# Kernel optimization log

Hardware: AMD Instinct MI355X
Metric: run time of the kernel (lower is better)

## Reference

```python
import jax, jax.numpy as jnp
import numpy as np

IN_CH = 256
HID = 64
HEADS = 3 * 0 + 4  # num_heads


def setup_inputs() -> dict:
    key = jax.random.key(0)
    ks = jax.random.split(key, 5)
    B, C, H, W = 2, IN_CH, 64, 64
    x = jax.random.normal(ks[0], (B, C, H, W), dtype=jnp.float32)
    # per-head embed conv (kernel 1 -> stored as [heads, 3*HID, C]); kaiming fan_out-ish scale
    w_embed = jax.random.normal(ks[1], (HEADS, 3 * HID, C), dtype=jnp.float32) * np.float32(np.sqrt(2.0 / (3 * HID)))
    b_embed = jnp.zeros((HEADS, 3 * HID), dtype=jnp.float32)
    # output ConvTranspose2d(hidden*heads -> C, kernel 1): weight [hidden*heads, C]
    w_out = jax.random.normal(ks[2], (HEADS * HID, C), dtype=jnp.float32) * np.float32(np.sqrt(2.0 / C))
    b_out = jnp.zeros((C,), dtype=jnp.float32)
    return {"x": x, "w_embed": w_embed, "b_embed": b_embed, "w_out": w_out, "b_out": b_out}


def reference(x, w_embed, b_embed, w_out, b_out):
    B, C, H, W = x.shape
    N = H * W
    nH = w_embed.shape[0]
    D = w_embed.shape[1] // 3
    scale = D ** -0.5
    # 1x1 embed conv per head: [B, nH, 3D, N]
    xf = x.reshape(B, C, N)
    qkv = jnp.einsum('bcn,hdc->bhdn', xf, w_embed) + b_embed[None, :, :, None]
    q, k, v = jnp.split(qkv, 3, axis=2)  # each [B, nH, D, N]
    attn = jnp.einsum('bhci,bhcj->bhij', q, k) * scale  # [B, nH, N, N]
    attn = jax.nn.softmax(attn, axis=-1)
    y = jnp.einsum('bhij,bhcj->bhci', attn, v)  # [B, nH, D, N]
    y = y.reshape(B, nH * D, N)
    # output 1x1 transposed conv (kernel 1 == plain 1x1 projection)
    out = jnp.einsum('bkn,kc->bcn', y, w_out) + b_out[None, :, None]
    out = out.reshape(B, C, H, W)
    return out + x  # residual
```

## Files before the change

### kernel.cpp

```cpp
#include <hip/hip_runtime.h>
#include <hip/hip_bf16.h>

#define NH   4
#define D_   64
#define N_   4096
#define C_   256
#define ME   768
#define QSCALE 0.18033688f

typedef float    f32x4  __attribute__((ext_vector_type(4)));
typedef float    f32x16 __attribute__((ext_vector_type(16)));
typedef _Float16 f16x8  __attribute__((ext_vector_type(8)));
typedef _Float16 f16x4  __attribute__((ext_vector_type(4)));
typedef unsigned int u32x2 __attribute__((ext_vector_type(2)));

#if defined(__has_builtin)
#if __has_builtin(__builtin_amdgcn_permlane32_swap)
#define HAVE_PERMLANE32_SWAP 1
#endif
#endif

__global__ __launch_bounds__(256) void prep_kernel(const float* __restrict__ x,
                                                   const float* __restrict__ w_out,
                                                   _Float16* __restrict__ xT,
                                                   _Float16* __restrict__ w_outT) {
    __shared__ float T[64][68];
    const int t = threadIdx.x, bx = blockIdx.x;
    if (bx < 512) {
        const int n0 = (bx & 63) * 64, c0 = ((bx >> 6) & 3) * 64, b = bx >> 8;
        const float* xp = x + ((size_t)b * C_ + c0) * N_ + n0;
        #pragma unroll
        for (int r = 0; r < 4; ++r) {
            int idx = r * 256 + t;
            int c = idx >> 4, ng = (idx & 15) * 4;
            *(f32x4*)&T[c][ng] = *(const f32x4*)(xp + (size_t)c * N_ + ng);
        }
        __syncthreads();
        _Float16* dp = xT + ((size_t)b * N_ + n0) * C_ + c0;
        #pragma unroll
        for (int r = 0; r < 2; ++r) {
            int idx = r * 256 + t;
            int n = idx >> 3, cg = (idx & 7) * 8;
            f16x8 v;
            #pragma unroll
            for (int j = 0; j < 8; ++j) v[j] = (_Float16)T[cg + j][n];
            *(f16x8*)(dp + (size_t)n * C_ + cg) = v;
        }
    } else {
        int tile = bx - 512;
        int tc = tile & 3, tk = tile >> 2;
        #pragma unroll
        for (int r = 0; r < 4; ++r) {
            int idx = r * 256 + t;
            int kl = idx >> 4, cl = (idx & 15) * 4;
            *(f32x4*)&T[kl][cl] = *(const f32x4*)(w_out + (size_t)(tk * 64 + kl) * C_ + tc * 64 + cl);
        }
        __syncthreads();
        #pragma unroll
        for (int r = 0; r < 2; ++r) {
            int idx = r * 256 + t;
            int cl = idx >> 3, kg = (idx & 7) * 8;
            f16x8 v;
            #pragma unroll
            for (int j = 0; j < 8; ++j) v[j] = (_Float16)T[kg + j][cl];
            *(f16x8*)(w_outT + (size_t)(tc * 64 + cl) * C_ + tk * 64 + kg) = v;
        }
    }
}

__global__ __launch_bounds__(256) void qkv_gemm(const _Float16* __restrict__ xT,
                                                const float* __restrict__ w_embed,
                                                const float* __restrict__ b_embed,
                                                _Float16* __restrict__ qT,
                                                _Float16* __restrict__ kT,
                                                _Float16* __restrict__ vB) {
    __shared__ __align__(16) union SM {
        struct { _Float16 A[64][40], X[64][40]; } s;
        float Os[64][68];
    } sm;
    const int n0 = blockIdx.x * 64, mt = blockIdx.y, b = blockIdx.z;
    const int m0 = mt * 64;
    const int t = threadIdx.x;
    const int lane = t & 63, w = t >> 6, quad = lane >> 4, l16 = lane & 15;
    const int srow = t >> 2, skoff = (t & 3) * 8;
    const int h = mt / 3, r3 = mt - h * 3;
    const float oscale = (r3 == 0) ? QSCALE : 1.0f;
    const float* ap = w_embed + (size_t)(m0 + srow) * C_ + skoff;
    const _Float16* xp = xT + ((size_t)b * N_ + n0 + srow) * C_ + skoff;
    f32x4 a0pre = *(const f32x4*)(ap);
    f32x4 a1pre = *(const f32x4*)(ap + 4);
    f16x8 xpre  = *(const f16x8*)(xp);
    f32x4 acc[4] = {};
    for (int k0 = 0; k0 < C_; k0 += 32) {
        __syncthreads();
        {
            f16x8 av = { (_Float16)a0pre[0], (_Float16)a0pre[1], (_Float16)a0pre[2], (_Float16)a0pre[3],
                         (_Float16)a1pre[0], (_Float16)a1pre[1], (_Float16)a1pre[2], (_Float16)a1pre[3] };
            *(f16x8*)&sm.s.A[srow][skoff] = av;
            *(f16x8*)&sm.s.X[srow][skoff] = xpre;
        }
        __syncthreads();
        if (k0 + 32 < C_) {
            a0pre = *(const f32x4*)(ap + k0 + 32);
            a1pre = *(const f32x4*)(ap + k0 + 36);
            xpre  = *(const f16x8*)(xp + k0 + 32);
        }
        f16x8 af = *(const f16x8*)&sm.s.A[w * 16 + l16][quad * 8];
        #pragma unroll
        for (int nb = 0; nb < 4; ++nb) {
            f16x8 bf = *(const f16x8*)&sm.s.X[nb * 16 + l16][quad * 8];
            acc[nb] = __builtin_amdgcn_mfma_f32_16x16x32_f16(af, bf, acc[nb], 0, 0, 0);
        }
    }
    float bias[4];
    #pragma unroll
    for (int rg = 0; rg < 4; ++rg) bias[rg] = b_embed[m0 + w * 16 + quad * 4 + rg];
    __syncthreads();
    #pragma unroll
    for (int nb = 0; nb < 4; ++nb)
        #pragma unroll
        for (int rg = 0; rg < 4; ++rg)
            sm.Os[w * 16 + quad * 4 + rg][nb * 16 + l16] = (acc[nb][rg] + bias[rg]) * oscale;
    __syncthreads();
    const int bh = b * NH + h;
    if (r3 < 2) {
        _Float16* dst = (r3 ? kT : qT) + ((size_t)bh * N_ + n0) * D_;
        #pragma unroll
        for (int r = 0; r < 2; ++r) {
            int idx = r * 256 + t;
            int n = idx >> 3, mg = (idx & 7) * 8;
            f16x8 v;
            #pragma unroll
            for (int j = 0; j < 8; ++j) v[j] = (_Float16)sm.Os[mg + j][n];
            *(f16x8*)(dst + (size_t)n * D_ + mg) = v;
        }
    } else {
        _Float16* dst = vB + (size_t)bh * D_ * N_ + n0;
        #pragma unroll
        for (int r = 0; r < 2; ++r) {
            int idx = r * 256 + t;
            int d = idx >> 3, ng = (idx & 7) * 8;
            f32x4 a = *(const f32x4*)&sm.Os[d][ng];
            f32x4 b2 = *(const f32x4*)&sm.Os[d][ng + 4];
            f16x8 v = { (_Float16)a[0], (_Float16)a[1], (_Float16)a[2], (_Float16)a[3],
                        (_Float16)b2[0], (_Float16)b2[1], (_Float16)b2[2], (_Float16)b2[3] };
            *(f16x8*)(dst + (size_t)d * N_ + ng) = v;
        }
    }
}

__global__ __launch_bounds__(256, 4) void attn_kernel(const _Float16* __restrict__ qT,
                                                      const _Float16* __restrict__ kT,
                                                      const _Float16* __restrict__ vB,
                                                      _Float16* __restrict__ opart,
                                                      float* __restrict__ mpart,
                                                      float* __restrict__ lpart,
                                                      int splog) {
    __shared__ __align__(16) union SM {
        struct { _Float16 K[2][64][76], V[2][64][76]; } s;
        _Float16 Os[128][76];
    } sm;
    const int t = threadIdx.x;
    const int nsp = 1 << splog;
    const int qt = blockIdx.x, h = blockIdx.y;
    const int b = blockIdx.z >> splog, s = blockIdx.z & (nsp - 1);
    const int bh = b * NH + h, sbh = s * 8 + bh;
    const _Float16* kp = kT + (size_t)bh * N_ * D_;
    const _Float16* vp = vB + (size_t)bh * D_ * N_;
    const int lane = t & 63, w = t >> 6, l32 = lane & 31, hl = lane >> 5;
    const int srow = t >> 3, scol = (t & 7) * 8;

    const _Float16* qp = qT + ((size_t)bh * N_ + qt * 128 + w * 32 + l32) * D_;
    f16x8 qf[4];
    #pragma unroll
    for (int kc = 0; kc < 4; ++kc) qf[kc] = *(const f16x8*)(qp + kc * 16 + hl * 8);

    f32x16 oacc0 = {}, oacc1 = {};
    float m_run = 0.f, l_run = 0.f;

    const int niter = 64 >> splog;
    const int jt_lo = s * niter, jt_hi = jt_lo + niter;
    f16x8 kpre[2], vpre[2];
    #pragma unroll
    for (int r = 0; r < 2; ++r) {
        int row = srow + r * 32;
        kpre[r] = *(const f16x8*)(kp + (size_t)(jt_lo * 64 + row) * D_ + scol);
        vpre[r] = *(const f16x8*)(vp + (size_t)row * N_ + jt_lo * 64 + scol);
    }

    int buf = 0;
    for (int jt = jt_lo; jt < jt_hi; ++jt, buf ^= 1) {
        #pragma unroll
        for (int r = 0; r < 2; ++r) {
            int row = srow + r * 32;
            *(f16x8*)&sm.s.K[buf][row][scol] = kpre[r];
            *(f16x8*)&sm.s.V[buf][row][scol] = vpre[r];
        }
        __syncthreads();
        if (jt + 1 < jt_hi) {
            #pragma unroll
            for (int r = 0; r < 2; ++r) {
                int row = srow + r * 32;
                kpre[r] = *(const f16x8*)(kp + (size_t)((jt + 1) * 64 + row) * D_ + scol);
                vpre[r] = *(const f16x8*)(vp + (size_t)row * N_ + (jt + 1) * 64 + scol);
            }
        }
        f32x16 sa0 = {}, sa1 = {};
        __builtin_amdgcn_s_setprio(1);
        #pragma unroll
        for (int kc = 0; kc < 4; ++kc) {
            f16x8 kf0 = *(const f16x8*)&sm.s.K[buf][l32][kc * 16 + hl * 8];
            sa0 = __builtin_amdgcn_mfma_f32_32x32x16_f16(kf0, qf[kc], sa0, 0, 0, 0);
            f16x8 kf1 = *(const f16x8*)&sm.s.K[buf][32 + l32][kc * 16 + hl * 8];
            sa1 = __builtin_amdgcn_mfma_f32_32x32x16_f16(kf1, qf[kc], sa1, 0, 0, 0);
        }
        __builtin_amdgcn_s_setprio(0);
        if (jt == jt_lo) {
            f32x16 mm;
            #pragma unroll
            for (int r = 0; r < 16; ++r) mm[r] = fmaxf(sa0[r], sa1[r]);
            f32x4 m4;
            #pragma unroll
            for (int r = 0; r < 4; ++r)
                m4[r] = fmaxf(fmaxf(mm[r], mm[r + 4]), fmaxf(mm[r + 8], mm[r + 12]));
            float mx = fmaxf(fmaxf(m4[0], m4[1]), fmaxf(m4[2], m4[3]));
            mx = fmaxf(mx, __shfl_xor(mx, 32));
            m_run = mx + 8.0f;
        }
        #pragma unroll
        for (int r = 0; r < 16; ++r) sa0[r] = __builtin_amdgcn_exp2f(sa0[r] - m_run);
        #pragma unroll
        for (int r = 0; r < 16; ++r) sa1[r] = __builtin_amdgcn_exp2f(sa1[r] - m_run);
        f32x16 sv = sa0 + sa1;
        f32x4 s4;
        #pragma unroll
        for (int r = 0; r < 4; ++r) s4[r] = (sv[r] + sv[r + 4]) + (sv[r + 8] + sv[r + 12]);
        float rs = (s4[0] + s4[1]) + (s4[2] + s4[3]);
        rs += __shfl_xor(rs, 32);
        l_run += rs;
#ifdef HAVE_PERMLANE32_SWAP
        #pragma unroll
        for (int jb = 0; jb < 2; ++jb) {
            const f32x16& sa = jb ? sa1 : sa0;
            #pragma unroll
            for (int kk = 0; kk < 2; ++kk) {
                unsigned int pa = __builtin_bit_cast(unsigned int,
                    __builtin_amdgcn_cvt_pkrtz(sa[kk * 8 + 0], sa[kk * 8 + 1]));
                unsigned int pb = __builtin_bit_cast(unsigned int,
                    __builtin_amdgcn_cvt_pkrtz(sa[kk * 8 + 2], sa[kk * 8 + 3]));
                unsigned int pc = __builtin_bit_cast(unsigned int,
                    __builtin_amdgcn_cvt_pkrtz(sa[kk * 8 + 4], sa[kk * 8 + 5]));
                unsigned int pd = __builtin_bit_cast(unsigned int,
                    __builtin_amdgcn_cvt_pkrtz(sa[kk * 8 + 6], sa[kk * 8 + 7]));
                u32x2 r0 = __builtin_amdgcn_permlane32_swap(pa, pc, false, false);
                u32x2 r1 = __builtin_amdgcn_permlane32_swap(pb, pd, false, false);
                union PF { unsigned int u[4]; f16x8 v; } pf;
                pf.u[0] = r0[0]; pf.u[1] = r1[0]; pf.u[2] = r0[1]; pf.u[3] = r1[1];
                const int vcol = jb * 32 + kk * 16 + hl * 8;
                f16x8 va  = *(const f16x8*)&sm.s.V[buf][l32][vcol];
                f16x8 vb2 = *(const f16x8*)&sm.s.V[buf][32 + l32][vcol];
                __builtin_amdgcn_s_setprio(1);
                oacc0 = __builtin_amdgcn_mfma_f32_32x32x16_f16(va, pf.v, oacc0, 0, 0, 0);
                oacc1 = __builtin_amdgcn_mfma_f32_32x32x16_f16(vb2, pf.v, oacc1, 0, 0, 0);
                __builtin_amdgcn_s_setprio(0);
            }
        }
#else
        #pragma unroll
        for (int jb = 0; jb < 2; ++jb) {
            const f32x16& sa = jb ? sa1 : sa0;
            union BU { f16x4 v; int d[2]; } bf[4];
            #pragma unroll
            for (int q = 0; q < 8; ++q)
                bf[q >> 1].d[q & 1] =
                    __builtin_bit_cast(int, __builtin_amdgcn_cvt_pkrtz(sa[2 * q], sa[2 * q + 1]));
            #pragma unroll
            for (int c = 0; c < 4; ++c) {
                const int vcol = jb * 32 + c * 8 + hl * 4;
                f16x4 va = *(const f16x4*)&sm.s.V[buf][l32][vcol];
                oacc0 = __builtin_amdgcn_mfma_f32_32x32x8f16(va, bf[c].v, oacc0, 0, 0, 0);
                f16x4 vb = *(const f16x4*)&sm.s.V[buf][32 + l32][vcol];
                oacc1 = __builtin_amdgcn_mfma_f32_32x32x8f16(vb, bf[c].v, oacc1, 0, 0, 0);
            }
        }
#endif
    }
    float linv = 1.f / l_run;
    if (hl == 0) {
        mpart[(size_t)sbh * N_ + qt * 128 + w * 32 + l32] = m_run;
        lpart[(size_t)sbh * N_ + qt * 128 + w * 32 + l32] = l_run;
    }
    __syncthreads();
    #pragma unroll
    for (int db = 0; db < 2; ++db) {
        const f32x16& oc = db ? oacc1 : oacc0;
        #pragma unroll
        for (int rq = 0; rq < 4; ++rq) {
            f16x4 pv = { (_Float16)(oc[rq * 4 + 0] * linv), (_Float16)(oc[rq * 4 + 1] * linv),
                         (_Float16)(oc[rq * 4 + 2] * linv), (_Float16)(oc[rq * 4 + 3] * linv) };
            *(f16x4*)&sm.Os[w * 32 + l32][db * 32 + rq * 8 + hl * 4] = pv;
        }
    }
    __syncthreads();
    _Float16* op = opart + ((size_t)sbh * N_ + qt * 128) * D_;
    #pragma unroll
    for (int r = 0; r < 4; ++r) {
        int idx = r * 256 + t;
        int i = idx >> 3, ch = (idx & 7) * 8;
        *(f16x8*)(op + (size_t)i * D_ + ch) = *(const f16x8*)&sm.Os[i][ch];
    }
}

__global__ __launch_bounds__(256) void projc_gemm(const _Float16* __restrict__ opart,
                                                  const float* __restrict__ mpart,
                                                  const float* __restrict__ lpart,
                                                  const _Float16* __restrict__ w_outT,
                                                  const float* __restrict__ b_out,
                                                  const float* __restrict__ x,
                                                  float* __restrict__ out) {
    __shared__ __align__(16) union SMP {
        struct {
            _Float16 Y[64][264];
            union { float W[4][64][4]; _Float16 A[128][40]; } u;
        } p;
        float Os[128][68];
    } sm;
    const int nt = blockIdx.x, chh = blockIdx.y, b = blockIdx.z;
    const int n0 = nt * 64, c0 = chh * 128;
    const int t = threadIdx.x;
    const int lane = t & 63, w = t >> 6, quad = lane >> 4, l16 = lane & 15;

    {
        const int nl = t & 63, hh = t >> 6;
        const int bh = b * NH + hh;
        float mv[4], lv[4];
        #pragma unroll
        for (int sI = 0; sI < 4; ++sI) {
            mv[sI] = mpart[(size_t)(sI * 8 + bh) * N_ + n0 + nl];
            lv[sI] = lpart[(size_t)(sI * 8 + bh) * N_ + n0 + nl];
        }
        float M = fmaxf(fmaxf(mv[0], mv[1]), fmaxf(mv[2], mv[3]));
        float ws[4], sum = 0.f;
        #pragma unroll
        for (int sI = 0; sI < 4; ++sI) {
            ws[sI] = __builtin_amdgcn_exp2f(mv[sI] - M) * lv[sI];
            sum += ws[sI];
        }
        float inv = 1.f / sum;
        #pragma unroll
        for (int sI = 0; sI < 4; ++sI) sm.p.u.W[hh][nl][sI] = ws[sI] * inv;
    }
    __syncthreads();

    #pragma unroll
    for (int it = 0; it < 8; ++it) {
        int idx = it * 256 + t;
        int n = idx >> 5, kg = (idx & 31) * 8;
        int hh = kg >> 6, d0 = kg & 63;
        const int bh = b * NH + hh;
        const float* Wn = &sm.p.u.W[hh][n][0];
        float accf[8] = {};
        #pragma unroll
        for (int sI = 0; sI < 4; ++sI) {
            f16x8 ov = *(const f16x8*)(opart + ((size_t)(sI * 8 + bh) * N_ + n0 + n) * D_ + d0);
            float wsv = Wn[sI];
            #pragma unroll
            for (int j = 0; j < 8; ++j) accf[j] += wsv * (float)ov[j];
        }
        f16x8 yv;
        #pragma unroll
        for (int j = 0; j < 8; ++j) yv[j] = (_Float16)accf[j];
        *(f16x8*)&sm.p.Y[n][kg] = yv;
    }
    __syncthreads();

    const int srow = t >> 1, skoff = (t & 1) * 16;
    const _Float16* ap = w_outT + (size_t)(c0 + srow) * C_ + skoff;
    f16x8 apre0 = *(const f16x8*)(ap);
    f16x8 apre1 = *(const f16x8*)(ap + 8);
    f32x4 acc[2][4] = {};
    for (int k0 = 0; k0 < C_; k0 += 32) {
        __syncthreads();
        *(f16x8*)&sm.p.u.A[srow][skoff]     = apre0;
        *(f16x8*)&sm.p.u.A[srow][skoff + 8] = apre1;
        __syncthreads();
        if (k0 + 32 < C_) {
            apre0 = *(const f16x8*)(ap + k0 + 32);
            apre1 = *(const f16x8*)(ap + k0 + 40);
        }
        #pragma unroll
        for (int cb = 0; cb < 2; ++cb) {
            f16x8 af = *(const f16x8*)&sm.p.u.A[w * 32 + cb * 16 + l16][quad * 8];
            #pragma unroll
            for (int nb = 0; nb < 4; ++nb) {
                f16x8 bf = *(const f16x8*)&sm.p.Y[nb * 16 + l16][k0 + quad * 8];
                acc[cb][nb] = __builtin_amdgcn_mfma_f32_16x16x32_f16(af, bf, acc[cb][nb], 0, 0, 0);
            }
        }
    }
    float bias[2][4];
    #pragma unroll
    for (int cb = 0; cb < 2; ++cb)
        #pragma unroll
        for (int rg = 0; rg < 4; ++rg)
            bias[cb][rg] = b_out[c0 + w * 32 + cb * 16 + quad * 4 + rg];
    __syncthreads();
    #pragma unroll
    for (int cb = 0; cb < 2; ++cb)
        #pragma unroll
        for (int nb = 0; nb < 4; ++nb)
            #pragma unroll
            for (int rg = 0; rg < 4; ++rg)
                sm.Os[w * 32 + cb * 16 + quad * 4 + rg][nb * 16 + l16] =
                    acc[cb][nb][rg] + bias[cb][rg];
    __syncthreads();
    const float* xp = x + ((size_t)b * C_ + c0) * N_ + n0;
    float* op = out + ((size_t)b * C_ + c0) * N_ + n0;
    #pragma unroll
    for (int r = 0; r < 8; ++r) {
        int idx = r * 256 + t;
        int c = idx >> 4, ng = (idx & 15) * 4;
        f32x4 v  = *(const f32x4*)&sm.Os[c][ng];
        f32x4 xv = *(const f32x4*)(xp + (size_t)c * N_ + ng);
        f32x4 o  = { v[0] + xv[0], v[1] + xv[1], v[2] + xv[2], v[3] + xv[3] };
        *(f32x4*)(op + (size_t)c * N_ + ng) = o;
    }
}

extern "C" void kernel_launch(void* const* d_in, const int* in_sizes, int n_in,
                              void* d_out, int out_size, void* d_ws, size_t ws_size,
                              hipStream_t stream) {
    const float* x       = (const float*)d_in[0];
    const float* w_embed = (const float*)d_in[1];
    const float* b_embed = (const float*)d_in[2];
    const float* w_out   = (const float*)d_in[3];
    const float* b_out   = (const float*)d_in[4];
    float* out = (float*)d_out;

    const int splog = 2;

    _Float16* base   = (_Float16*)d_ws;
    _Float16* xT     = base;
    _Float16* w_outT = base + 2293760;
    _Float16* qT     = base + 2359296;
    _Float16* kT     = base + 4456448;
    _Float16* vB     = base + 6553600;
    _Float16* opart  = base + 8650752;
    float*    mpart  = (float*)(opart + (size_t)4 * 8 * N_ * D_);
    float*    lpart  = mpart + (size_t)4 * 8 * N_;

    prep_kernel<<<dim3(528, 1, 1), 256, 0, stream>>>(x, w_out, xT, w_outT);
    qkv_gemm   <<<dim3(64, 12, 2), 256, 0, stream>>>(xT, w_embed, b_embed, qT, kT, vB);
    attn_kernel<<<dim3(32, 4, 2 << splog), 256, 0, stream>>>(qT, kT, vB, opart, mpart, lpart, splog);
    projc_gemm <<<dim3(64, 2, 2),  256, 0, stream>>>(opart, mpart, lpart, w_outT, b_out, x, out);
}
```

Measured before the change: 149.2 us.

## Single-buffer attention LDS, drop setprio, and allow 8-way KV split

The attention kernel's K/V shared-memory tiles go from double-buffered to single-buffered, with an extra barrier before each tile store. This roughly halves LDS use per block, which could let more blocks run at once per CU. The s_setprio hints around the MFMA sections are removed. When the workspace is large enough, the KV dimension is split 8 ways instead of 4, doubling attention grid parallelism, and the projection kernel is templated on the split count to merge more partial results. The extra barrier, the lost load/compute overlap and the larger partial-output traffic could offset these gains.

```diff
diff --git a/kernel.cpp b/kernel.cpp
--- a/kernel.cpp
+++ b/kernel.cpp
@@ -157,7 +157,7 @@
                                                       float* __restrict__ lpart,
                                                       int splog) {
     __shared__ __align__(16) union SM {
-        struct { _Float16 K[2][64][76], V[2][64][76]; } s;
+        struct { _Float16 K[64][76], V[64][76]; } s;
         _Float16 Os[128][76];
     } sm;
     const int t = threadIdx.x;
@@ -188,13 +188,13 @@
         vpre[r] = *(const f16x8*)(vp + (size_t)row * N_ + jt_lo * 64 + scol);
     }
 
-    int buf = 0;
-    for (int jt = jt_lo; jt < jt_hi; ++jt, buf ^= 1) {
+    for (int jt = jt_lo; jt < jt_hi; ++jt) {
+        __syncthreads();
         #pragma unroll
         for (int r = 0; r < 2; ++r) {
             int row = srow + r * 32;
-            *(f16x8*)&sm.s.K[buf][row][scol] = kpre[r];
-            *(f16x8*)&sm.s.V[buf][row][scol] = vpre[r];
+            *(f16x8*)&sm.s.K[row][scol] = kpre[r];
+            *(f16x8*)&sm.s.V[row][scol] = vpre[r];
         }
         __syncthreads();
         if (jt + 1 < jt_hi) {
@@ -206,15 +206,13 @@
             }
         }
         f32x16 sa0 = {}, sa1 = {};
-        __builtin_amdgcn_s_setprio(1);
         #pragma unroll
         for (int kc = 0; kc < 4; ++kc) {
-            f16x8 kf0 = *(const f16x8*)&sm.s.K[buf][l32][kc * 16 + hl * 8];
+            f16x8 kf0 = *(const f16x8*)&sm.s.K[l32][kc * 16 + hl * 8];
             sa0 = __builtin_amdgcn_mfma_f32_32x32x16_f16(kf0, qf[kc], sa0, 0, 0, 0);
-            f16x8 kf1 = *(const f16x8*)&sm.s.K[buf][32 + l32][kc * 16 + hl * 8];
+            f16x8 kf1 = *(const f16x8*)&sm.s.K[32 + l32][kc * 16 + hl * 8];
             sa1 = __builtin_amdgcn_mfma_f32_32x32x16_f16(kf1, qf[kc], sa1, 0, 0, 0);
         }
-        __builtin_amdgcn_s_setprio(0);
         if (jt == jt_lo) {
             f32x16 mm;
             #pragma unroll
@@ -257,12 +255,10 @@
                 union PF { unsigned int u[4]; f16x8 v; } pf;
                 pf.u[0] = r0[0]; pf.u[1] = r1[0]; pf.u[2] = r0[1]; pf.u[3] = r1[1];
                 const int vcol = jb * 32 + kk * 16 + hl * 8;
-                f16x8 va  = *(const f16x8*)&sm.s.V[buf][l32][vcol];
-                f16x8 vb2 = *(const f16x8*)&sm.s.V[buf][32 + l32][vcol];
-                __builtin_amdgcn_s_setprio(1);
+                f16x8 va  = *(const f16x8*)&sm.s.V[l32][vcol];
+                f16x8 vb2 = *(const f16x8*)&sm.s.V[32 + l32][vcol];
                 oacc0 = __builtin_amdgcn_mfma_f32_32x32x16_f16(va, pf.v, oacc0, 0, 0, 0);
                 oacc1 = __builtin_amdgcn_mfma_f32_32x32x16_f16(vb2, pf.v, oacc1, 0, 0, 0);
-                __builtin_amdgcn_s_setprio(0);
             }
         }
 #else
@@ -277,9 +273,9 @@
             #pragma unroll
             for (int c = 0; c < 4; ++c) {
                 const int vcol = jb * 32 + c * 8 + hl * 4;
-                f16x4 va = *(const f16x4*)&sm.s.V[buf][l32][vcol];
+                f16x4 va = *(const f16x4*)&sm.s.V[l32][vcol];
                 oacc0 = __builtin_amdgcn_mfma_f32_32x32x8f16(va, bf[c].v, oacc0, 0, 0, 0);
-                f16x4 vb = *(const f16x4*)&sm.s.V[buf][32 + l32][vcol];
+                f16x4 vb = *(const f16x4*)&sm.s.V[32 + l32][vcol];
                 oacc1 = __builtin_amdgcn_mfma_f32_32x32x8f16(vb, bf[c].v, oacc1, 0, 0, 0);
             }
         }
@@ -311,6 +307,7 @@
     }
 }
 
+template<int NSP>
 __global__ __launch_bounds__(256) void projc_gemm(const _Float16* __restrict__ opart,
                                                   const float* __restrict__ mpart,
                                                   const float* __restrict__ lpart,
@@ -321,7 +318,7 @@
     __shared__ __align__(16) union SMP {
         struct {
             _Float16 Y[64][264];
-            union { float W[4][64][4]; _Float16 A[128][40]; } u;
+            union { float W[4][64][NSP]; _Float16 A[128][40]; } u;
         } p;
         float Os[128][68];
     } sm;
@@ -333,22 +330,24 @@
     {
         const int nl = t & 63, hh = t >> 6;
         const int bh = b * NH + hh;
-        float mv[4], lv[4];
-        #pragma unroll
-        for (int sI = 0; sI < 4; ++sI) {
+        float mv[NSP], lv[NSP];
+        #pragma unroll
+        for (int sI = 0; sI < NSP; ++sI) {
             mv[sI] = mpart[(size_t)(sI * 8 + bh) * N_ + n0 + nl];
             lv[sI] = lpart[(size_t)(sI * 8 + bh) * N_ + n0 + nl];
         }
-        float M = fmaxf(fmaxf(mv[0], mv[1]), fmaxf(mv[2], mv[3]));
-        float ws[4], sum = 0.f;
-        #pragma unroll
-        for (int sI = 0; sI < 4; ++sI) {
+        float M = mv[0];
+        #pragma unroll
+        for (int sI = 1; sI < NSP; ++sI) M = fmaxf(M, mv[sI]);
+        float ws[NSP], sum = 0.f;
+        #pragma unroll
+        for (int sI = 0; sI < NSP; ++sI) {
             ws[sI] = __builtin_amdgcn_exp2f(mv[sI] - M) * lv[sI];
             sum += ws[sI];
         }
         float inv = 1.f / sum;
         #pragma unroll
-        for (int sI = 0; sI < 4; ++sI) sm.p.u.W[hh][nl][sI] = ws[sI] * inv;
+        for (int sI = 0; sI < NSP; ++sI) sm.p.u.W[hh][nl][sI] = ws[sI] * inv;
     }
     __syncthreads();
 
@@ -361,7 +360,7 @@
         const float* Wn = &sm.p.u.W[hh][n][0];
         float accf[8] = {};
         #pragma unroll
-        for (int sI = 0; sI < 4; ++sI) {
+        for (int sI = 0; sI < NSP; ++sI) {
             f16x8 ov = *(const f16x8*)(opart + ((size_t)(sI * 8 + bh) * N_ + n0 + n) * D_ + d0);
             float wsv = Wn[sI];
             #pragma unroll
@@ -437,7 +436,9 @@
     const float* b_out   = (const float*)d_in[4];
     float* out = (float*)d_out;
 
-    const int splog = 2;
+    const bool big = ws_size >= 53500000ull;
+    const int splog = big ? 3 : 2;
+    const size_t nsp = (size_t)1 << splog;
 
     _Float16* base   = (_Float16*)d_ws;
     _Float16* xT     = base;
@@ -446,11 +447,14 @@
     _Float16* kT     = base + 4456448;
     _Float16* vB     = base + 6553600;
     _Float16* opart  = base + 8650752;
-    float*    mpart  = (float*)(opart + (size_t)4 * 8 * N_ * D_);
-    float*    lpart  = mpart + (size_t)4 * 8 * N_;
+    float*    mpart  = (float*)(opart + nsp * 8 * N_ * D_);
+    float*    lpart  = mpart + nsp * 8 * N_;
 
     prep_kernel<<<dim3(528, 1, 1), 256, 0, stream>>>(x, w_out, xT, w_outT);
     qkv_gemm   <<<dim3(64, 12, 2), 256, 0, stream>>>(xT, w_embed, b_embed, qT, kT, vB);
     attn_kernel<<<dim3(32, 4, 2 << splog), 256, 0, stream>>>(qT, kT, vB, opart, mpart, lpart, splog);
-    projc_gemm <<<dim3(64, 2, 2),  256, 0, stream>>>(opart, mpart, lpart, w_outT, b_out, x, out);
+    if (big)
+        projc_gemm<8><<<dim3(64, 2, 2), 256, 0, stream>>>(opart, mpart, lpart, w_outT, b_out, x, out);
+    else
+        projc_gemm<4><<<dim3(64, 2, 2), 256, 0, stream>>>(opart, mpart, lpart, w_outT, b_out, x, out);
 }
```

Result: slower. 152.9 us (+2.5%).
